# Performance work log

Measured on AMD Instinct MI355X. Metric: run time of the kernel, lower is better.

Reference implementation:

```python
import jax, jax.numpy as jnp
import numpy as np

NUM_SEGMENTS = 512


def setup_inputs() -> dict:
    key = jax.random.key(0)
    k1, k2, k3, k4, k5, k6 = jax.random.split(key, 6)
    hidden = 256
    num_words = 200000
    x = jax.random.normal(k1, (num_words, hidden), dtype=jnp.float32)
    batch = jnp.sort(jax.random.randint(k2, (num_words,), 0, NUM_SEGMENTS, dtype=jnp.int64))
    s = 1.0 / np.sqrt(hidden)
    W1 = jax.random.uniform(k3, (hidden, hidden), minval=-s, maxval=s, dtype=jnp.float32)
    b1 = jax.random.uniform(k4, (hidden,), minval=-s, maxval=s, dtype=jnp.float32)
    W2 = jax.random.uniform(k5, (hidden, hidden), minval=-s, maxval=s, dtype=jnp.float32)
    b2 = jax.random.uniform(k6, (hidden,), minval=-s, maxval=s, dtype=jnp.float32)
    return {"x": x, "batch": batch, "W1": W1, "b1": b1, "W2": W2, "b2": b2}


def reference(x, batch, W1, b1, W2, b2):
    # embedding transform: Linear + ReLU  [N, H]
    h = jax.nn.relu(x @ W1.T + b1)
    # feature attention: Linear + Sigmoid, gate multiply
    att = jax.nn.sigmoid(h @ W2.T + b2)
    g = h * att  # attended features [N, H]

    seg = batch.astype(jnp.int32)
    counts = jax.ops.segment_sum(jnp.ones((g.shape[0],), g.dtype), seg,
                                 num_segments=NUM_SEGMENTS)  # [B]
    seg_sum = jax.ops.segment_sum(g, seg, num_segments=NUM_SEGMENTS)  # [B, H]
    seg_max = jax.ops.segment_max(g, seg, num_segments=NUM_SEGMENTS)  # [B, H]

    nonempty = (counts > 0)[:, None]
    max_pool = jnp.where(nonempty, seg_max, 0.0)  # torch leaves zeros for empty graphs
    mean_pool = jnp.where(nonempty, seg_sum / jnp.maximum(counts, 1.0)[:, None], 0.0)
    return jnp.concatenate([max_pool, mean_pool], axis=1)  # [B, 2H]
```

## Files before the change

kernel.cpp:

```cpp
#include <hip/hip_runtime.h>

#define H 256

typedef short bf16x8 __attribute__((ext_vector_type(8)));
typedef float f32x4  __attribute__((ext_vector_type(4)));

__device__ __forceinline__ unsigned int f2bf(float f) {
    unsigned int u = __float_as_uint(f);
    return (u + 0x7fffu + ((u >> 16) & 1u)) >> 16;
}
__device__ __forceinline__ int clampseg(int s) { return s < 0 ? 0 : (s > 511 ? 511 : s); }

__global__ void conv_w_kernel(const float* __restrict__ W1, const float* __restrict__ W2,
                              unsigned short* __restrict__ W1b, unsigned short* __restrict__ W2b) {
    int i = blockIdx.x * 256 + threadIdx.x;
    W1b[i] = (unsigned short)f2bf(W1[i]);
    W2b[i] = (unsigned short)f2bf(W2[i]);
}

__global__ __launch_bounds__(1024, 4) void fused_v5(
    const float* __restrict__ x, const int* __restrict__ batch,
    const unsigned short* __restrict__ W1b, const float* __restrict__ b1,
    const unsigned short* __restrict__ W2b, const float* __restrict__ b2,
    float* __restrict__ out, int* __restrict__ counts, int nchunks)
{
    __shared__ __align__(16) unsigned short xl[2][64][264];
    __shared__ __align__(16) unsigned short hl[64][264];

    const int tid  = threadIdx.x;
    const int wave = tid >> 6, lane = tid & 63;
    const int r = lane & 15, q = lane >> 4;
    const int col = wave * 16 + r;

    const int b  = blockIdx.x;
    const int c0 = (int)(((long long)b       * nchunks) >> 8);
    const int c1 = (int)(((long long)(b + 1) * nchunks) >> 8);
    if (c0 >= c1) return;

    const float bias1 = b1[col];
    const float bias2 = b2[col];

    float accs[4] = {0.f, 0.f, 0.f, 0.f};
    float accm[4] = {0.f, 0.f, 0.f, 0.f};
    int wb = clampseg(batch[c0 * 64]);

#define FLUSH_SLOTS()                                                              \
    do {                                                                           \
        _Pragma("unroll")                                                          \
        for (int s = 0; s < 4; ++s) {                                              \
            float sv = accs[s];                                                    \
            float mv = accm[s];                                                    \
            sv += __shfl_xor(sv, 16, 64);                                          \
            sv += __shfl_xor(sv, 32, 64);                                          \
            mv = fmaxf(mv, __shfl_xor(mv, 16, 64));                                \
            mv = fmaxf(mv, __shfl_xor(mv, 32, 64));                                \
            if (q == 0 && (sv != 0.f || mv != 0.f)) {                              \
                const int seg = clampseg(wb + s);                                  \
                atomicAdd(&out[(size_t)seg * 512 + 256 + col], sv);                \
                atomicMax((unsigned int*)&out[(size_t)seg * 512 + col],            \
                          __float_as_uint(mv));                                    \
            }                                                                      \
            accs[s] = 0.f; accm[s] = 0.f;                                          \
        }                                                                          \
    } while (0)

    {
        const float* src = x + (size_t)c0 * 64 * H;
#pragma unroll
        for (int i = 0; i < 2; ++i) {
            const int ch = tid + (i << 10);
            const float4 lo = *(const float4*)(src + ch * 8);
            const float4 hi = *(const float4*)(src + ch * 8 + 4);
            bf16x8 v;
            v[0] = (short)f2bf(lo.x); v[1] = (short)f2bf(lo.y);
            v[2] = (short)f2bf(lo.z); v[3] = (short)f2bf(lo.w);
            v[4] = (short)f2bf(hi.x); v[5] = (short)f2bf(hi.y);
            v[6] = (short)f2bf(hi.z); v[7] = (short)f2bf(hi.w);
            *(bf16x8*)&xl[0][ch >> 5][(ch & 31) * 8] = v;
        }
    }
    __syncthreads();

    int cur = 0;
    for (int c = c0; c < c1; ++c) {
        const int rowbase = c * 64;
        const bool have_next = (c + 1 < c1);

        float4 st0, st1, st2, st3;
        if (have_next) {
            const float* src = x + (size_t)(c + 1) * 64 * H;
            const int ch0 = tid, ch1 = tid + 1024;
            st0 = *(const float4*)(src + ch0 * 8);
            st1 = *(const float4*)(src + ch0 * 8 + 4);
            st2 = *(const float4*)(src + ch1 * 8);
            st3 = *(const float4*)(src + ch1 * 8 + 4);
        }

        float hv[16];
        {
            bf16x8 w1f[8];
            const unsigned short* wrow = W1b + (size_t)col * H + q * 8;
#pragma unroll
            for (int kk = 0; kk < 8; ++kk)
                w1f[kk] = *(const bf16x8*)(wrow + kk * 32);
#pragma unroll
            for (int rg = 0; rg < 4; ++rg) {
                f32x4 a = (f32x4){0.f, 0.f, 0.f, 0.f};
#pragma unroll
                for (int kk = 0; kk < 8; ++kk) {
                    bf16x8 af = *(const bf16x8*)&xl[cur][rg * 16 + r][kk * 32 + q * 8];
                    a = __builtin_amdgcn_mfma_f32_16x16x32_bf16(af, w1f[kk], a, 0, 0, 0);
                }
#pragma unroll
                for (int e = 0; e < 4; ++e) {
                    float h = a[e] + bias1;
                    h = h > 0.f ? h : 0.f;
                    hv[rg * 4 + e] = h;
                    hl[rg * 16 + q * 4 + e][col] = (unsigned short)f2bf(h);
                }
            }
        }
        __syncthreads();

        if (have_next) {
            bf16x8 v;
            v[0] = (short)f2bf(st0.x); v[1] = (short)f2bf(st0.y);
            v[2] = (short)f2bf(st0.z); v[3] = (short)f2bf(st0.w);
            v[4] = (short)f2bf(st1.x); v[5] = (short)f2bf(st1.y);
            v[6] = (short)f2bf(st1.z); v[7] = (short)f2bf(st1.w);
            *(bf16x8*)&xl[cur ^ 1][tid >> 5][(tid & 31) * 8] = v;
            const int ch1 = tid + 1024;
            v[0] = (short)f2bf(st2.x); v[1] = (short)f2bf(st2.y);
            v[2] = (short)f2bf(st2.z); v[3] = (short)f2bf(st2.w);
            v[4] = (short)f2bf(st3.x); v[5] = (short)f2bf(st3.y);
            v[6] = (short)f2bf(st3.z); v[7] = (short)f2bf(st3.w);
            *(bf16x8*)&xl[cur ^ 1][ch1 >> 5][(ch1 & 31) * 8] = v;
        }

        {
            bf16x8 w2f[8];
            const unsigned short* wrow = W2b + (size_t)col * H + q * 8;
#pragma unroll
            for (int kk = 0; kk < 8; ++kk)
                w2f[kk] = *(const bf16x8*)(wrow + kk * 32);
#pragma unroll
            for (int rg = 0; rg < 4; ++rg) {
                const int r0 = rowbase + rg * 16;

                if (wave == 0 && lane < 16)
                    atomicAdd(&counts[clampseg(batch[r0 + lane])], 1);

                const int hi_seg = clampseg(batch[r0 + 15]);
                if (hi_seg - wb > 3) {
                    FLUSH_SLOTS();
                    wb = clampseg(batch[r0]);
                }

                f32x4 a = (f32x4){0.f, 0.f, 0.f, 0.f};
#pragma unroll
                for (int kk = 0; kk < 8; ++kk) {
                    bf16x8 af = *(const bf16x8*)&hl[rg * 16 + r][kk * 32 + q * 8];
                    a = __builtin_amdgcn_mfma_f32_16x16x32_bf16(af, w2f[kk], a, 0, 0, 0);
                }
#pragma unroll
                for (int e = 0; e < 4; ++e) {
                    float t   = a[e] + bias2;
                    float att = 1.f / (1.f + __expf(-t));
                    float gg  = hv[rg * 4 + e] * att;
                    const int d = clampseg(batch[r0 + q * 4 + e]) - wb;
#pragma unroll
                    for (int s = 0; s < 4; ++s)
                        if (d == s) { accs[s] += gg; accm[s] = fmaxf(accm[s], gg); }
                    if (d < 0 || d > 3) {
                        const int seg = clampseg(wb + d);
                        atomicAdd(&out[(size_t)seg * 512 + 256 + col], gg);
                        atomicMax((unsigned int*)&out[(size_t)seg * 512 + col],
                                  __float_as_uint(gg));
                    }
                }
            }
        }
        __syncthreads();
        cur ^= 1;
    }

    FLUSH_SLOTS();
#undef FLUSH_SLOTS
}

__global__ void finalize_kernel(float* __restrict__ out, const int* __restrict__ counts) {
    const int b = blockIdx.x;
    const int c = threadIdx.x;
    const int cnt = counts[b];
    float s = out[(size_t)b * 512 + 256 + c];
    out[(size_t)b * 512 + 256 + c] = cnt > 0 ? s / (float)cnt : 0.0f;
}

extern "C" void kernel_launch(void* const* d_in, const int* in_sizes, int n_in,
                              void* d_out, int out_size, void* d_ws, size_t ws_size,
                              hipStream_t stream) {
    const float* x     = (const float*)d_in[0];
    const int*   batch = (const int*)d_in[1];
    const float* W1    = (const float*)d_in[2];
    const float* b1    = (const float*)d_in[3];
    const float* W2    = (const float*)d_in[4];
    const float* b2    = (const float*)d_in[5];
    float* out = (float*)d_out;

    unsigned short* W1b    = (unsigned short*)d_ws;
    unsigned short* W2b    = W1b + 65536;
    int*            counts = (int*)(W2b + 65536);

    const int Nrows   = in_sizes[0] / H;
    const int nchunks = Nrows / 64;

    hipMemsetAsync(d_out, 0, (size_t)out_size * sizeof(float), stream);
    hipMemsetAsync(counts, 0, 512 * sizeof(int), stream);
    conv_w_kernel<<<256, 256, 0, stream>>>(W1, W2, W1b, W2b);
    fused_v5<<<256, 1024, 0, stream>>>(x, batch, W1b, b1, W2b, b2, out, counts, nchunks);
    finalize_kernel<<<512, 256, 0, stream>>>(out, counts);
}
```

Measured before the change: 393.2 us.

## Halve row chunk, double grid, add uniform-segment fast path and MFMA priority

Rows are now processed in chunks of 32 instead of 64, which halves the LDS and register footprint. The grid doubles to 512 blocks with a launch bound of 8, so two blocks can share each CU and hide memory latency. When all 16 rows in a group belong to one segment, they are reduced in registers and counted with a single atomic; otherwise the per-element slot path is used. s_setprio is raised around the MFMA loops, and the counts memset is folded into the weight-conversion kernel. The atomic fallback for segments outside the slot window is removed, which relies on batch being sorted. The tighter register budget may also cause spills.

```diff
diff --git a/kernel.cpp b/kernel.cpp
--- a/kernel.cpp
+++ b/kernel.cpp
@@ -1,6 +1,7 @@
 #include <hip/hip_runtime.h>
 
 #define H 256
+#define CH 32
 
 typedef short bf16x8 __attribute__((ext_vector_type(8)));
 typedef float f32x4  __attribute__((ext_vector_type(4)));
@@ -12,20 +13,25 @@
 __device__ __forceinline__ int clampseg(int s) { return s < 0 ? 0 : (s > 511 ? 511 : s); }
 
 __global__ void conv_w_kernel(const float* __restrict__ W1, const float* __restrict__ W2,
-                              unsigned short* __restrict__ W1b, unsigned short* __restrict__ W2b) {
+                              unsigned short* __restrict__ W1b, unsigned short* __restrict__ W2b,
+                              int* __restrict__ counts) {
     int i = blockIdx.x * 256 + threadIdx.x;
     W1b[i] = (unsigned short)f2bf(W1[i]);
     W2b[i] = (unsigned short)f2bf(W2[i]);
-}
-
-__global__ __launch_bounds__(1024, 4) void fused_v5(
+    if (blockIdx.x == 0 && threadIdx.x < 256) {
+        counts[threadIdx.x] = 0;
+        counts[threadIdx.x + 256] = 0;
+    }
+}
+
+__global__ __launch_bounds__(1024, 8) void fused_v6(
     const float* __restrict__ x, const int* __restrict__ batch,
     const unsigned short* __restrict__ W1b, const float* __restrict__ b1,
     const unsigned short* __restrict__ W2b, const float* __restrict__ b2,
     float* __restrict__ out, int* __restrict__ counts, int nchunks)
 {
-    __shared__ __align__(16) unsigned short xl[2][64][264];
-    __shared__ __align__(16) unsigned short hl[64][264];
+    __shared__ __align__(16) unsigned short xl[2][CH][264];
+    __shared__ __align__(16) unsigned short hl[CH][264];
 
     const int tid  = threadIdx.x;
     const int wave = tid >> 6, lane = tid & 63;
@@ -33,8 +39,8 @@
     const int col = wave * 16 + r;
 
     const int b  = blockIdx.x;
-    const int c0 = (int)(((long long)b       * nchunks) >> 8);
-    const int c1 = (int)(((long long)(b + 1) * nchunks) >> 8);
+    const int c0 = (int)(((long long)b       * nchunks) >> 9);
+    const int c1 = (int)(((long long)(b + 1) * nchunks) >> 9);
     if (c0 >= c1) return;
 
     const float bias1 = b1[col];
@@ -42,7 +48,7 @@
 
     float accs[4] = {0.f, 0.f, 0.f, 0.f};
     float accm[4] = {0.f, 0.f, 0.f, 0.f};
-    int wb = clampseg(batch[c0 * 64]);
+    int wb = clampseg(batch[c0 * CH]);
 
 #define FLUSH_SLOTS()                                                              \
     do {                                                                           \
@@ -65,38 +71,31 @@
     } while (0)
 
     {
-        const float* src = x + (size_t)c0 * 64 * H;
-#pragma unroll
-        for (int i = 0; i < 2; ++i) {
-            const int ch = tid + (i << 10);
-            const float4 lo = *(const float4*)(src + ch * 8);
-            const float4 hi = *(const float4*)(src + ch * 8 + 4);
-            bf16x8 v;
-            v[0] = (short)f2bf(lo.x); v[1] = (short)f2bf(lo.y);
-            v[2] = (short)f2bf(lo.z); v[3] = (short)f2bf(lo.w);
-            v[4] = (short)f2bf(hi.x); v[5] = (short)f2bf(hi.y);
-            v[6] = (short)f2bf(hi.z); v[7] = (short)f2bf(hi.w);
-            *(bf16x8*)&xl[0][ch >> 5][(ch & 31) * 8] = v;
-        }
+        const float* src = x + (size_t)c0 * CH * H + tid * 8;
+        const float4 lo = *(const float4*)(src);
+        const float4 hi = *(const float4*)(src + 4);
+        bf16x8 v;
+        v[0] = (short)f2bf(lo.x); v[1] = (short)f2bf(lo.y);
+        v[2] = (short)f2bf(lo.z); v[3] = (short)f2bf(lo.w);
+        v[4] = (short)f2bf(hi.x); v[5] = (short)f2bf(hi.y);
+        v[6] = (short)f2bf(hi.z); v[7] = (short)f2bf(hi.w);
+        *(bf16x8*)&xl[0][tid >> 5][(tid & 31) * 8] = v;
     }
     __syncthreads();
 
     int cur = 0;
     for (int c = c0; c < c1; ++c) {
-        const int rowbase = c * 64;
+        const int rowbase = c * CH;
         const bool have_next = (c + 1 < c1);
 
-        float4 st0, st1, st2, st3;
+        float4 st0, st1;
         if (have_next) {
-            const float* src = x + (size_t)(c + 1) * 64 * H;
-            const int ch0 = tid, ch1 = tid + 1024;
-            st0 = *(const float4*)(src + ch0 * 8);
-            st1 = *(const float4*)(src + ch0 * 8 + 4);
-            st2 = *(const float4*)(src + ch1 * 8);
-            st3 = *(const float4*)(src + ch1 * 8 + 4);
-        }
-
-        float hv[16];
+            const float* src = x + (size_t)(c + 1) * CH * H + tid * 8;
+            st0 = *(const float4*)(src);
+            st1 = *(const float4*)(src + 4);
+        }
+
+        float hv[8];
         {
             bf16x8 w1f[8];
             const unsigned short* wrow = W1b + (size_t)col * H + q * 8;
@@ -104,13 +103,15 @@
             for (int kk = 0; kk < 8; ++kk)
                 w1f[kk] = *(const bf16x8*)(wrow + kk * 32);
 #pragma unroll
-            for (int rg = 0; rg < 4; ++rg) {
+            for (int rg = 0; rg < 2; ++rg) {
                 f32x4 a = (f32x4){0.f, 0.f, 0.f, 0.f};
+                __builtin_amdgcn_s_setprio(1);
 #pragma unroll
                 for (int kk = 0; kk < 8; ++kk) {
                     bf16x8 af = *(const bf16x8*)&xl[cur][rg * 16 + r][kk * 32 + q * 8];
                     a = __builtin_amdgcn_mfma_f32_16x16x32_bf16(af, w1f[kk], a, 0, 0, 0);
                 }
+                __builtin_amdgcn_s_setprio(0);
 #pragma unroll
                 for (int e = 0; e < 4; ++e) {
                     float h = a[e] + bias1;
@@ -129,12 +130,6 @@
             v[4] = (short)f2bf(st1.x); v[5] = (short)f2bf(st1.y);
             v[6] = (short)f2bf(st1.z); v[7] = (short)f2bf(st1.w);
             *(bf16x8*)&xl[cur ^ 1][tid >> 5][(tid & 31) * 8] = v;
-            const int ch1 = tid + 1024;
-            v[0] = (short)f2bf(st2.x); v[1] = (short)f2bf(st2.y);
-            v[2] = (short)f2bf(st2.z); v[3] = (short)f2bf(st2.w);
-            v[4] = (short)f2bf(st3.x); v[5] = (short)f2bf(st3.y);
-            v[6] = (short)f2bf(st3.z); v[7] = (short)f2bf(st3.w);
-            *(bf16x8*)&xl[cur ^ 1][ch1 >> 5][(ch1 & 31) * 8] = v;
         }
 
         {
@@ -144,38 +139,55 @@
             for (int kk = 0; kk < 8; ++kk)
                 w2f[kk] = *(const bf16x8*)(wrow + kk * 32);
 #pragma unroll
-            for (int rg = 0; rg < 4; ++rg) {
+            for (int rg = 0; rg < 2; ++rg) {
                 const int r0 = rowbase + rg * 16;
 
-                if (wave == 0 && lane < 16)
-                    atomicAdd(&counts[clampseg(batch[r0 + lane])], 1);
-
-                const int hi_seg = clampseg(batch[r0 + 15]);
-                if (hi_seg - wb > 3) {
+                const int sA = __builtin_amdgcn_readfirstlane(clampseg(batch[r0]));
+                const int sB = __builtin_amdgcn_readfirstlane(clampseg(batch[r0 + 15]));
+                const bool unig = (sA == sB);
+
+                if (wave == 0) {
+                    if (unig) { if (lane == 0) atomicAdd(&counts[sA], 16); }
+                    else if (lane < 16) atomicAdd(&counts[clampseg(batch[r0 + lane])], 1);
+                }
+
+                if (sB - wb > 3) {
                     FLUSH_SLOTS();
-                    wb = clampseg(batch[r0]);
+                    wb = sA;
                 }
 
                 f32x4 a = (f32x4){0.f, 0.f, 0.f, 0.f};
+                __builtin_amdgcn_s_setprio(1);
 #pragma unroll
                 for (int kk = 0; kk < 8; ++kk) {
                     bf16x8 af = *(const bf16x8*)&hl[rg * 16 + r][kk * 32 + q * 8];
                     a = __builtin_amdgcn_mfma_f32_16x16x32_bf16(af, w2f[kk], a, 0, 0, 0);
                 }
+                __builtin_amdgcn_s_setprio(0);
+
+                float g4[4];
 #pragma unroll
                 for (int e = 0; e < 4; ++e) {
                     float t   = a[e] + bias2;
                     float att = 1.f / (1.f + __expf(-t));
-                    float gg  = hv[rg * 4 + e] * att;
-                    const int d = clampseg(batch[r0 + q * 4 + e]) - wb;
-#pragma unroll
-                    for (int s = 0; s < 4; ++s)
-                        if (d == s) { accs[s] += gg; accm[s] = fmaxf(accm[s], gg); }
-                    if (d < 0 || d > 3) {
-                        const int seg = clampseg(wb + d);
-                        atomicAdd(&out[(size_t)seg * 512 + 256 + col], gg);
-                        atomicMax((unsigned int*)&out[(size_t)seg * 512 + col],
-                                  __float_as_uint(gg));
+                    g4[e] = hv[rg * 4 + e] * att;
+                }
+
+                if (unig) {
+                    const int d = sA - wb;
+                    float s = (g4[0] + g4[1]) + (g4[2] + g4[3]);
+                    float m = fmaxf(fmaxf(g4[0], g4[1]), fmaxf(g4[2], g4[3]));
+                    if      (d == 0) { accs[0] += s; accm[0] = fmaxf(accm[0], m); }
+                    else if (d == 1) { accs[1] += s; accm[1] = fmaxf(accm[1], m); }
+                    else if (d == 2) { accs[2] += s; accm[2] = fmaxf(accm[2], m); }
+                    else             { accs[3] += s; accm[3] = fmaxf(accm[3], m); }
+                } else {
+#pragma unroll
+                    for (int e = 0; e < 4; ++e) {
+                        const int d = clampseg(batch[r0 + q * 4 + e]) - wb;
+#pragma unroll
+                        for (int s = 0; s < 4; ++s)
+                            if (d == s) { accs[s] += g4[e]; accm[s] = fmaxf(accm[s], g4[e]); }
                     }
                 }
             }
@@ -212,11 +224,10 @@
     int*            counts = (int*)(W2b + 65536);
 
     const int Nrows   = in_sizes[0] / H;
-    const int nchunks = Nrows / 64;
+    const int nchunks = Nrows / CH;
 
     hipMemsetAsync(d_out, 0, (size_t)out_size * sizeof(float), stream);
-    hipMemsetAsync(counts, 0, 512 * sizeof(int), stream);
-    conv_w_kernel<<<256, 256, 0, stream>>>(W1, W2, W1b, W2b);
-    fused_v5<<<256, 1024, 0, stream>>>(x, batch, W1b, b1, W2b, b2, out, counts, nchunks);
+    conv_w_kernel<<<256, 256, 0, stream>>>(W1, W2, W1b, W2b, counts);
+    fused_v6<<<512, 1024, 0, stream>>>(x, batch, W1b, b1, W2b, b2, out, counts, nchunks);
     finalize_kernel<<<512, 256, 0, stream>>>(out, counts);
 }
```

Result: slower. 647.0 us (+64.5%).
